# Optimization experiments

Hardware: AMD Instinct MI355X
Metric: run time of the kernel (lower is better)

The kernel has to match this reference:

```python
import jax, jax.numpy as jnp
import numpy as np

D_MODEL = 1024
NUM_HEADS = 16
D_K = D_MODEL // NUM_HEADS
LN_EPS = 1e-5


def setup_inputs() -> dict:
    key = jax.random.key(0)
    ks = jax.random.split(key, 10)
    s = 1.0 / np.sqrt(D_MODEL)
    x = jax.random.normal(ks[0], (4, 2048, D_MODEL), dtype=jnp.float32)
    Wq = jax.random.normal(ks[1], (D_MODEL, D_MODEL), dtype=jnp.float32) * s
    bq = jnp.zeros((D_MODEL,), dtype=jnp.float32)
    Wk = jax.random.normal(ks[2], (D_MODEL, D_MODEL), dtype=jnp.float32) * s
    bk = jnp.zeros((D_MODEL,), dtype=jnp.float32)
    Wv = jax.random.normal(ks[3], (D_MODEL, D_MODEL), dtype=jnp.float32) * s
    bv = jnp.zeros((D_MODEL,), dtype=jnp.float32)
    Wo = jax.random.normal(ks[4], (D_MODEL, D_MODEL), dtype=jnp.float32) * s
    bo = jnp.zeros((D_MODEL,), dtype=jnp.float32)
    gamma = jnp.ones((D_MODEL,), dtype=jnp.float32)
    beta = jnp.zeros((D_MODEL,), dtype=jnp.float32)
    return {"x": x, "Wq": Wq, "bq": bq, "Wk": Wk, "bk": bk,
            "Wv": Wv, "bv": bv, "Wo": Wo, "bo": bo,
            "gamma": gamma, "beta": beta}


def reference(x, Wq, bq, Wk, bk, Wv, bv, Wo, bo, gamma, beta):
    # x: [b, s, d]; torch Linear: y = x @ W.T + b. Dropout is identity (eval).
    b, s, d = x.shape
    h, dk = NUM_HEADS, D_K

    def proj(W, bias):  # [b, s, h, dk] -> [b, h, s, dk]
        return (jnp.einsum('bsd,ed->bse', x, W) + bias).reshape(b, s, h, dk).transpose(0, 2, 1, 3)

    Q, K, V = proj(Wq, bq), proj(Wk, bk), proj(Wv, bv)
    scores = jnp.einsum('bhqk,bhsk->bhqs', Q, K) / jnp.sqrt(jnp.float32(dk))
    attn = jax.nn.softmax(scores, axis=-1)
    ctx = jnp.einsum('bhqs,bhsk->bhqk', attn, V)  # [b, h, s, dk]
    ctx = ctx.transpose(0, 2, 1, 3).reshape(b, s, d)
    out = jnp.einsum('bsd,ed->bse', ctx, Wo) + bo
    y = out + x  # residual
    mu = jnp.mean(y, axis=-1, keepdims=True)
    var = jnp.mean(jnp.square(y - mu), axis=-1, keepdims=True)
    return (y - mu) * jax.lax.rsqrt(var + LN_EPS) * gamma + beta
```

## Files before the change

### kernel.cpp

```cpp
#include <hip/hip_runtime.h>

typedef unsigned short u16;
typedef unsigned int   u32;
typedef float f32x4 __attribute__((ext_vector_type(4)));
typedef short s16x8 __attribute__((ext_vector_type(8)));

#define D_MODEL 1024
#define NHEADS  16
#define DK      64
#define SEQ     2048
#define BATCH   4
#define MROWS   (BATCH * SEQ)

#define C2 0.18033688011112042f

#if __has_builtin(__builtin_amdgcn_exp2f)
#define EXP2(x) __builtin_amdgcn_exp2f(x)
#else
#define EXP2(x) exp2f(x)
#endif

#define GL16(gp, lp) __builtin_amdgcn_global_load_lds( \
    (const __attribute__((address_space(1))) u32*)(gp), \
    (__attribute__((address_space(3))) u32*)(lp), 16, 0, 0)

__device__ __forceinline__ u16 f2b(float f) {
    u32 u = __builtin_bit_cast(u32, f);
    u32 r = (u + 0x7fffu + ((u >> 16) & 1u)) >> 16;
    return (u16)r;
}
__device__ __forceinline__ u32 pack2_trunc(float a, float b) {
    return __builtin_amdgcn_perm(__builtin_bit_cast(u32, b),
                                 __builtin_bit_cast(u32, a), 0x07060302u);
}

__global__ __launch_bounds__(256)
void cvt_all(const float* __restrict__ x,  const float* __restrict__ wq,
             const float* __restrict__ wk, const float* __restrict__ wv,
             const float* __restrict__ wo,
             u16* __restrict__ xb, u16* __restrict__ wqb, u16* __restrict__ wkb,
             u16* __restrict__ wvb, u16* __restrict__ wob)
{
    const int i = blockIdx.x * 256 + threadIdx.x;
    const float* src; u16* dst; int off;
    if (i < 2097152) { src = x; dst = xb; off = i; }
    else {
        const int j = i - 2097152;
        const int w = j >> 18;
        off = j & 262143;
        if      (w == 0) { src = wq; dst = wqb; }
        else if (w == 1) { src = wk; dst = wkb; }
        else if (w == 2) { src = wv; dst = wvb; }
        else             { src = wo; dst = wob; }
    }
    const float4 v = reinterpret_cast<const float4*>(src)[off];
    u32 lo = (u32)f2b(v.x) | ((u32)f2b(v.y) << 16);
    u32 hi = (u32)f2b(v.z) | ((u32)f2b(v.w) << 16);
    reinterpret_cast<uint2*>(dst)[off] = make_uint2(lo, hi);
}

#define QBM 256
#define QBN 128
#define BK 32
#define KITER (D_MODEL / BK)

__global__ __launch_bounds__(512, 4)
void gemm_qkv(const u16* __restrict__ A,
              const u16* __restrict__ Wq, const u16* __restrict__ Wk,
              const u16* __restrict__ Wv,
              const float* __restrict__ bq, const float* __restrict__ bk,
              const float* __restrict__ bv,
              u16* __restrict__ Qb, u16* __restrict__ Kb, u16* __restrict__ VtB)
{
    __shared__ __align__(16) u16 As[2][8192];
    __shared__ __align__(16) u16 Bs[2][4096];
    const int t    = threadIdx.x;
    const int lane = t & 63;
    const int w    = t >> 6;
    const int wm = w >> 1, wn = w & 1;
    const int sel = blockIdx.x >> 3;
    const int n0  = (blockIdx.x & 7) * QBN;
    const int m0  = blockIdx.y * QBM;
    const int quad = lane >> 4;
    const int rlo  = lane & 15;

    const u16* W = (sel == 0) ? Wq : (sel == 1) ? Wk : Wv;
    const float* bias = (sel == 0) ? bq : (sel == 1) ? bk : bv;

    const int srow = w * 16 + rlo;
    const long aoff0 = (long)(m0 + srow) * D_MODEL + quad * 8;
    const long aoff1 = aoff0 + (long)128 * D_MODEL;
    const long boff  = (long)(n0 + srow) * D_MODEL + quad * 8;
    const int dstw = w * 512 + lane * 8;

    f32x4 acc[4][4];
    #pragma unroll
    for (int i = 0; i < 4; i++)
        #pragma unroll
        for (int j = 0; j < 4; j++)
            acc[i][j] = (f32x4){0.f, 0.f, 0.f, 0.f};

    GL16(A + aoff0, &As[0][dstw]);
    GL16(A + aoff1, &As[0][dstw + 4096]);
    GL16(W + boff,  &Bs[0][dstw]);

    for (int it = 0; it < KITER; it++) {
        const int cur = it & 1;
        __syncthreads();
        if (it + 1 < KITER) {
            const int k0 = (it + 1) * BK;
            const int nxt = cur ^ 1;
            GL16(A + aoff0 + k0, &As[nxt][dstw]);
            GL16(A + aoff1 + k0, &As[nxt][dstw + 4096]);
            GL16(W + boff + k0,  &Bs[nxt][dstw]);
        }
        s16x8 af[4], bf[4];
        #pragma unroll
        for (int i = 0; i < 4; i++)
            af[i] = *reinterpret_cast<const s16x8*>(&As[cur][(wm * 4 + i) * 512 + lane * 8]);
        #pragma unroll
        for (int j = 0; j < 4; j++)
            bf[j] = *reinterpret_cast<const s16x8*>(&Bs[cur][(wn * 4 + j) * 512 + lane * 8]);
        #pragma unroll
        for (int i = 0; i < 4; i++)
            #pragma unroll
            for (int j = 0; j < 4; j++)
                acc[i][j] = __builtin_amdgcn_mfma_f32_16x16x32_bf16(af[i], bf[j], acc[i][j], 0, 0, 0);
    }

    if (sel == 2) {
        #pragma unroll
        for (int i = 0; i < 4; i++) {
            #pragma unroll
            for (int j = 0; j < 4; j++) {
                const int gm0 = m0 + wm * 64 + i * 16 + quad * 4;
                const int gn  = n0 + wn * 64 + j * 16 + rlo;
                const float bvx = bias[gn];
                const int bb = gm0 >> 11, s = gm0 & 2047;
                const int h = gn >> 6, d = gn & 63;
                uint2 wv2;
                wv2.x = (u32)f2b(acc[i][j][0] + bvx) | ((u32)f2b(acc[i][j][1] + bvx) << 16);
                wv2.y = (u32)f2b(acc[i][j][2] + bvx) | ((u32)f2b(acc[i][j][3] + bvx) << 16);
                *reinterpret_cast<uint2*>(VtB + ((long)((bb * 16 + h) * 64 + d)) * 2048 + s) = wv2;
            }
        }
    } else {
        u16* outp = (sel == 0) ? Qb : Kb;
        const float scale = (sel == 0) ? C2 : 1.0f;
        #pragma unroll
        for (int i = 0; i < 4; i++)
            #pragma unroll
            for (int j = 0; j < 4; j++)
                #pragma unroll
                for (int r = 0; r < 4; r++) {
                    const int gm = m0 + wm * 64 + i * 16 + quad * 4 + r;
                    const int gn = n0 + wn * 64 + j * 16 + rlo;
                    outp[(long)gm * D_MODEL + gn] = f2b((acc[i][j][r] + bias[gn]) * scale);
                }
    }
}

#define BM 128
#define BN 128

__global__ __launch_bounds__(256, 3)
void gemm_o(const u16* __restrict__ A, const u16* __restrict__ W,
            const float* __restrict__ bias, const float* __restrict__ resid,
            float* __restrict__ outF)
{
    __shared__ __align__(16) u16 As[2][4096];
    __shared__ __align__(16) u16 Bs[2][4096];
    const int t    = threadIdx.x;
    const int lane = t & 63;
    const int wave = t >> 6;
    const int wr = wave >> 1, wc = wave & 1;
    const int n0  = blockIdx.x * BN;
    const int m0  = blockIdx.y * BM;
    const int quad = lane >> 4;
    const int rlo  = lane & 15;

    const int srow0 = wave * 16 + rlo;
    const int scol  = quad * 8;
    const long aoff0 = (long)(m0 + srow0) * D_MODEL + scol;
    const long aoff1 = aoff0 + (long)64 * D_MODEL;
    const long boff0 = (long)(n0 + srow0) * D_MODEL + scol;
    const long boff1 = boff0 + (long)64 * D_MODEL;
    const int dst = wave * 512 + lane * 8;

    f32x4 acc[4][4];
    #pragma unroll
    for (int i = 0; i < 4; i++)
        #pragma unroll
        for (int j = 0; j < 4; j++)
            acc[i][j] = (f32x4){0.f, 0.f, 0.f, 0.f};

    GL16(A + aoff0, &As[0][dst]);
    GL16(A + aoff1, &As[0][dst + 2048]);
    GL16(W + boff0, &Bs[0][dst]);
    GL16(W + boff1, &Bs[0][dst + 2048]);

    for (int it = 0; it < KITER; it++) {
        const int cur = it & 1;
        __syncthreads();
        if (it + 1 < KITER) {
            const int k0 = (it + 1) * BK;
            const int nxt = cur ^ 1;
            GL16(A + aoff0 + k0, &As[nxt][dst]);
            GL16(A + aoff1 + k0, &As[nxt][dst + 2048]);
            GL16(W + boff0 + k0, &Bs[nxt][dst]);
            GL16(W + boff1 + k0, &Bs[nxt][dst + 2048]);
        }
        s16x8 af[4], bf[4];
        #pragma unroll
        for (int i = 0; i < 4; i++)
            af[i] = *reinterpret_cast<const s16x8*>(&As[cur][(wr * 4 + i) * 512 + lane * 8]);
        #pragma unroll
        for (int j = 0; j < 4; j++)
            bf[j] = *reinterpret_cast<const s16x8*>(&Bs[cur][(wc * 4 + j) * 512 + lane * 8]);
        #pragma unroll
        for (int i = 0; i < 4; i++)
            #pragma unroll
            for (int j = 0; j < 4; j++)
                acc[i][j] = __builtin_amdgcn_mfma_f32_16x16x32_bf16(af[i], bf[j], acc[i][j], 0, 0, 0);
    }

    #pragma unroll
    for (int i = 0; i < 4; i++)
        #pragma unroll
        for (int j = 0; j < 4; j++)
            #pragma unroll
            for (int r = 0; r < 4; r++) {
                const int gm = m0 + wr * 64 + i * 16 + quad * 4 + r;
                const int gn = n0 + wc * 64 + j * 16 + rlo;
                outF[(long)gm * D_MODEL + gn] =
                    acc[i][j][r] + bias[gn] + resid[(long)gm * D_MODEL + gn];
            }
}

#define PSTR 72

__global__ __launch_bounds__(256, 3)
void flash_attn_mfma(const u16* __restrict__ Qg, const u16* __restrict__ Kg,
                     const u16* __restrict__ VtG, u16* __restrict__ C)
{
    __shared__ __align__(16) u16 smem[20992];
    u16* KsB   = &smem[4608];
    u16* VtBuf = &smem[12800];

    const int t    = threadIdx.x;
    const int lane = t & 63;
    const int wave = t >> 6;
    const int quad = lane >> 4;
    const int rlo  = lane & 15;
    const int qt = blockIdx.x, h = blockIdx.y, b = blockIdx.z;
    const long colbase = (long)h * DK;
    const long rowb    = (long)b * SEQ;
    const long qrow0   = rowb + (long)qt * 128;
    const u16* kg    = Kg + rowb * D_MODEL + colbase;
    const u16* vbase = VtG + (long)(b * 16 + h) * 64 * 2048;
    u16* myPs = &smem[wave * 1152];

    const long koff = (long)(wave * 16 + rlo) * D_MODEL + quad * 8;
    const long voff = (long)(wave * 16 + rlo) * 2048 + quad * 8;
    const int  dkv  = wave * 512 + lane * 8;

    GL16(kg + koff,         &KsB[dkv]);
    GL16(kg + koff + 32,    &KsB[dkv + 2048]);
    GL16(vbase + voff,      &VtBuf[dkv]);
    GL16(vbase + voff + 32, &VtBuf[dkv + 2048]);

    s16x8 bfq[2][2];
    #pragma unroll
    for (int mi = 0; mi < 2; mi++)
        #pragma unroll
        for (int ks = 0; ks < 2; ks++)
            bfq[mi][ks] = *reinterpret_cast<const s16x8*>(
                Qg + (qrow0 + wave * 32 + mi * 16 + rlo) * D_MODEL +
                colbase + ks * 32 + quad * 8);

    s16x8 ones;
    #pragma unroll
    for (int e = 0; e < 8; e++) ones[e] = (short)0x3F80;

    float m2[2] = {-INFINITY, -INFINITY};
    f32x4 o[2][4], o5[2];
    #pragma unroll
    for (int mi = 0; mi < 2; mi++) {
        o5[mi] = (f32x4){0.f, 0.f, 0.f, 0.f};
        #pragma unroll
        for (int db = 0; db < 4; db++)
            o[mi][db] = (f32x4){0.f, 0.f, 0.f, 0.f};
    }

    for (int kt = 0; kt < SEQ / 64; kt++) {
        const int cur = kt & 1;
        __syncthreads();
        if (kt + 1 < SEQ / 64) {
            const long kv0 = (long)(kt + 1) * 64;
            const int nb = cur ^ 1;
            GL16(kg + kv0 * D_MODEL + koff,      &KsB[nb * 4096 + dkv]);
            GL16(kg + kv0 * D_MODEL + koff + 32, &KsB[nb * 4096 + dkv + 2048]);
            GL16(vbase + kv0 + voff,             &VtBuf[nb * 4096 + dkv]);
            GL16(vbase + kv0 + voff + 32,        &VtBuf[nb * 4096 + dkv + 2048]);
        }
        const u16* Ks  = &KsB[cur * 4096];
        const u16* Vts = &VtBuf[cur * 4096];

        s16x8 afk[2][4], bfv[4][2];
        #pragma unroll
        for (int ks = 0; ks < 2; ks++)
            #pragma unroll
            for (int kb = 0; kb < 4; kb++)
                afk[ks][kb] = *reinterpret_cast<const s16x8*>(
                    &Ks[ks * 2048 + kb * 512 + lane * 8]);
        #pragma unroll
        for (int db = 0; db < 4; db++)
            #pragma unroll
            for (int ks = 0; ks < 2; ks++)
                bfv[db][ks] = *reinterpret_cast<const s16x8*>(
                    &Vts[ks * 2048 + db * 512 + lane * 8]);

        #pragma unroll
        for (int mi = 0; mi < 2; mi++) {
            f32x4 sc[4];
            #pragma unroll
            for (int kb = 0; kb < 4; kb++) sc[kb] = (f32x4){0.f, 0.f, 0.f, 0.f};
            #pragma unroll
            for (int ks = 0; ks < 2; ks++)
                #pragma unroll
                for (int kb = 0; kb < 4; kb++)
                    sc[kb] = __builtin_amdgcn_mfma_f32_16x16x32_bf16(
                        afk[ks][kb], bfq[mi][ks], sc[kb], 0, 0, 0);

            float rmax = sc[0][0];
            #pragma unroll
            for (int kb = 0; kb < 4; kb++)
                #pragma unroll
                for (int r = 0; r < 4; r++)
                    rmax = fmaxf(rmax, sc[kb][r]);
            rmax = fmaxf(rmax, __shfl_xor(rmax, 16));
            rmax = fmaxf(rmax, __shfl_xor(rmax, 32));
            const float mnew = fmaxf(m2[mi], rmax);
            const float alpha = EXP2(m2[mi] - mnew);
            m2[mi] = mnew;
            #pragma unroll
            for (int kb = 0; kb < 4; kb++) {
                float p0 = EXP2(sc[kb][0] - mnew);
                float p1 = EXP2(sc[kb][1] - mnew);
                float p2 = EXP2(sc[kb][2] - mnew);
                float p3 = EXP2(sc[kb][3] - mnew);
                uint2 wv2;
                wv2.x = pack2_trunc(p0, p1);
                wv2.y = pack2_trunc(p2, p3);
                *reinterpret_cast<uint2*>(&myPs[rlo * PSTR + kb * 16 + quad * 4]) = wv2;
            }

            s16x8 afp[2];
            #pragma unroll
            for (int ks = 0; ks < 2; ks++)
                afp[ks] = *reinterpret_cast<const s16x8*>(
                    &myPs[rlo * PSTR + ks * 32 + quad * 8]);

            #pragma unroll
            for (int r = 0; r < 4; r++) {
                const float ar = __shfl(alpha, (lane & 48) | (quad * 4 + r));
                #pragma unroll
                for (int db = 0; db < 4; db++)
                    o[mi][db][r] *= ar;
                o5[mi][r] *= ar;
            }

            #pragma unroll
            for (int ks = 0; ks < 2; ks++) {
                #pragma unroll
                for (int db = 0; db < 4; db++)
                    o[mi][db] = __builtin_amdgcn_mfma_f32_16x16x32_bf16(
                        afp[ks], bfv[db][ks], o[mi][db], 0, 0, 0);
                o5[mi] = __builtin_amdgcn_mfma_f32_16x16x32_bf16(
                    afp[ks], ones, o5[mi], 0, 0, 0);
            }
        }
    }

    #pragma unroll
    for (int mi = 0; mi < 2; mi++)
        #pragma unroll
        for (int r = 0; r < 4; r++) {
            const float inv = 1.f / o5[mi][r];
            const long grow = qrow0 + wave * 32 + mi * 16 + quad * 4 + r;
            #pragma unroll
            for (int db = 0; db < 4; db++)
                C[grow * D_MODEL + colbase + db * 16 + rlo] = f2b(o[mi][db][r] * inv);
        }
}

__global__ __launch_bounds__(256)
void ln_inplace(float* __restrict__ Y, const float* __restrict__ gamma,
                const float* __restrict__ beta)
{
    const int row = blockIdx.x, t = threadIdx.x;
    float4 v = reinterpret_cast<float4*>(Y + (long)row * D_MODEL)[t];
    float s  = v.x + v.y + v.z + v.w;
    float ss = v.x * v.x + v.y * v.y + v.z * v.z + v.w * v.w;
    #pragma unroll
    for (int off = 32; off > 0; off >>= 1) {
        s  += __shfl_down(s, off, 64);
        ss += __shfl_down(ss, off, 64);
    }
    __shared__ float rs[4], rss[4];
    const int lane = t & 63, w = t >> 6;
    if (lane == 0) { rs[w] = s; rss[w] = ss; }
    __syncthreads();
    const float tot  = rs[0] + rs[1] + rs[2] + rs[3];
    const float tot2 = rss[0] + rss[1] + rss[2] + rss[3];
    const float mu   = tot * (1.f / D_MODEL);
    const float var  = tot2 * (1.f / D_MODEL) - mu * mu;
    const float rstd = rsqrtf(var + 1e-5f);
    const float4 g  = reinterpret_cast<const float4*>(gamma)[t];
    const float4 bb = reinterpret_cast<const float4*>(beta)[t];
    v.x = (v.x - mu) * rstd * g.x + bb.x;
    v.y = (v.y - mu) * rstd * g.y + bb.y;
    v.z = (v.z - mu) * rstd * g.z + bb.z;
    v.w = (v.w - mu) * rstd * g.w + bb.w;
    reinterpret_cast<float4*>(Y + (long)row * D_MODEL)[t] = v;
}

extern "C" void kernel_launch(void* const* d_in, const int* in_sizes, int n_in,
                              void* d_out, int out_size, void* d_ws, size_t ws_size,
                              hipStream_t stream)
{
    const float* x     = (const float*)d_in[0];
    const float* Wq    = (const float*)d_in[1];
    const float* bq    = (const float*)d_in[2];
    const float* Wk    = (const float*)d_in[3];
    const float* bk    = (const float*)d_in[4];
    const float* Wv    = (const float*)d_in[5];
    const float* bv    = (const float*)d_in[6];
    const float* Wo    = (const float*)d_in[7];
    const float* bo    = (const float*)d_in[8];
    const float* gamma = (const float*)d_in[9];
    const float* beta  = (const float*)d_in[10];
    float* out = (float*)d_out;

    u16* ws  = (u16*)d_ws;
    u16* xb  = ws;
    u16* Wqb = xb  + (size_t)MROWS * D_MODEL;
    u16* Wkb = Wqb + (size_t)D_MODEL * D_MODEL;
    u16* Wvb = Wkb + (size_t)D_MODEL * D_MODEL;
    u16* Wob = Wvb + (size_t)D_MODEL * D_MODEL;
    u16* Qb  = Wob + (size_t)D_MODEL * D_MODEL;
    u16* Kb  = Qb  + (size_t)MROWS * D_MODEL;
    u16* VtB = Kb  + (size_t)MROWS * D_MODEL;
    u16* Cb  = VtB + (size_t)MROWS * D_MODEL;

    cvt_all<<<12288, 256, 0, stream>>>(x, Wq, Wk, Wv, Wo, xb, Wqb, Wkb, Wvb, Wob);

    gemm_qkv<<<dim3(24, 32), 512, 0, stream>>>(xb, Wqb, Wkb, Wvb, bq, bk, bv,
                                               Qb, Kb, VtB);

    flash_attn_mfma<<<dim3(SEQ / 128, NHEADS, BATCH), 256, 0, stream>>>(Qb, Kb, VtB, Cb);

    gemm_o<<<dim3(8, 64), 256, 0, stream>>>(Cb, Wob, bo, x, out);

    ln_inplace<<<MROWS, 256, 0, stream>>>(out, gamma, beta);
}
```

Baseline: 358.8 us.

## Swizzle P tile in LDS, lazy softmax rescale, setprio, raise occupancy

The padded P staging buffer (stride 72) becomes an XOR-swizzled 64-wide layout. This shrinks LDS enough to raise launch bounds from 3 to 4 blocks per SM, and each 16-byte read becomes two 8-byte reads. The online-softmax rescale of the accumulators is skipped unless some row max grows by more than 8 in log2 units, which saves multiplies and shuffles but lets unnormalized probabilities grow up to 2^8. s_setprio is also raised around the MFMA bursts to favour matrix issue across waves.

```diff
diff --git a/kernel.cpp b/kernel.cpp
--- a/kernel.cpp
+++ b/kernel.cpp
@@ -4,6 +4,7 @@
 typedef unsigned int   u32;
 typedef float f32x4 __attribute__((ext_vector_type(4)));
 typedef short s16x8 __attribute__((ext_vector_type(8)));
+typedef u32 u32x4 __attribute__((ext_vector_type(4)));
 
 #define D_MODEL 1024
 #define NHEADS  16
@@ -237,28 +238,28 @@
             }
 }
 
-#define PSTR 72
-
-__global__ __launch_bounds__(256, 3)
+
+__global__ __launch_bounds__(256, 4)
 void flash_attn_mfma(const u16* __restrict__ Qg, const u16* __restrict__ Kg,
                      const u16* __restrict__ VtG, u16* __restrict__ C)
 {
-    __shared__ __align__(16) u16 smem[20992];
-    u16* KsB   = &smem[4608];
-    u16* VtBuf = &smem[12800];
+    __shared__ __align__(16) u16 smem[20480];
+    u16* KsB   = &smem[4096];
+    u16* VtBuf = &smem[12288];
 
     const int t    = threadIdx.x;
     const int lane = t & 63;
     const int wave = t >> 6;
     const int quad = lane >> 4;
     const int rlo  = lane & 15;
+    const int swz  = rlo << 2;
     const int qt = blockIdx.x, h = blockIdx.y, b = blockIdx.z;
     const long colbase = (long)h * DK;
     const long rowb    = (long)b * SEQ;
     const long qrow0   = rowb + (long)qt * 128;
     const u16* kg    = Kg + rowb * D_MODEL + colbase;
     const u16* vbase = VtG + (long)(b * 16 + h) * 64 * 2048;
-    u16* myPs = &smem[wave * 1152];
+    u16* myPs = &smem[wave * 1024];
 
     const long koff = (long)(wave * 16 + rlo) * D_MODEL + quad * 8;
     const long voff = (long)(wave * 16 + rlo) * 2048 + quad * 8;
@@ -325,12 +326,14 @@
             f32x4 sc[4];
             #pragma unroll
             for (int kb = 0; kb < 4; kb++) sc[kb] = (f32x4){0.f, 0.f, 0.f, 0.f};
+            __builtin_amdgcn_s_setprio(1);
             #pragma unroll
             for (int ks = 0; ks < 2; ks++)
                 #pragma unroll
                 for (int kb = 0; kb < 4; kb++)
                     sc[kb] = __builtin_amdgcn_mfma_f32_16x16x32_bf16(
                         afk[ks][kb], bfq[mi][ks], sc[kb], 0, 0, 0);
+            __builtin_amdgcn_s_setprio(0);
 
             float rmax = sc[0][0];
             #pragma unroll
@@ -340,36 +343,47 @@
                     rmax = fmaxf(rmax, sc[kb][r]);
             rmax = fmaxf(rmax, __shfl_xor(rmax, 16));
             rmax = fmaxf(rmax, __shfl_xor(rmax, 32));
-            const float mnew = fmaxf(m2[mi], rmax);
-            const float alpha = EXP2(m2[mi] - mnew);
-            m2[mi] = mnew;
+
+            if (!__all(rmax <= m2[mi] + 8.0f)) {
+                const float mnew = fmaxf(m2[mi], rmax);
+                const float alpha = EXP2(m2[mi] - mnew);
+                m2[mi] = mnew;
+                #pragma unroll
+                for (int r = 0; r < 4; r++) {
+                    const float ar = __shfl(alpha, (lane & 48) | (quad * 4 + r));
+                    #pragma unroll
+                    for (int db = 0; db < 4; db++)
+                        o[mi][db][r] *= ar;
+                    o5[mi][r] *= ar;
+                }
+            }
+            const float mcur = m2[mi];
             #pragma unroll
             for (int kb = 0; kb < 4; kb++) {
-                float p0 = EXP2(sc[kb][0] - mnew);
-                float p1 = EXP2(sc[kb][1] - mnew);
-                float p2 = EXP2(sc[kb][2] - mnew);
-                float p3 = EXP2(sc[kb][3] - mnew);
+                float p0 = EXP2(sc[kb][0] - mcur);
+                float p1 = EXP2(sc[kb][1] - mcur);
+                float p2 = EXP2(sc[kb][2] - mcur);
+                float p3 = EXP2(sc[kb][3] - mcur);
                 uint2 wv2;
                 wv2.x = pack2_trunc(p0, p1);
                 wv2.y = pack2_trunc(p2, p3);
-                *reinterpret_cast<uint2*>(&myPs[rlo * PSTR + kb * 16 + quad * 4]) = wv2;
+                *reinterpret_cast<uint2*>(
+                    &myPs[rlo * 64 + ((kb * 16 + quad * 4) ^ swz)]) = wv2;
             }
 
             s16x8 afp[2];
             #pragma unroll
-            for (int ks = 0; ks < 2; ks++)
-                afp[ks] = *reinterpret_cast<const s16x8*>(
-                    &myPs[rlo * PSTR + ks * 32 + quad * 8]);
-
-            #pragma unroll
-            for (int r = 0; r < 4; r++) {
-                const float ar = __shfl(alpha, (lane & 48) | (quad * 4 + r));
-                #pragma unroll
-                for (int db = 0; db < 4; db++)
-                    o[mi][db][r] *= ar;
-                o5[mi][r] *= ar;
-            }
-
+            for (int ks = 0; ks < 2; ks++) {
+                const uint2 lo = *reinterpret_cast<const uint2*>(
+                    &myPs[rlo * 64 + ((ks * 32 + quad * 8) ^ swz)]);
+                const uint2 hi = *reinterpret_cast<const uint2*>(
+                    &myPs[rlo * 64 + ((ks * 32 + quad * 8 + 4) ^ swz)]);
+                u32x4 tv;
+                tv.x = lo.x; tv.y = lo.y; tv.z = hi.x; tv.w = hi.y;
+                afp[ks] = __builtin_bit_cast(s16x8, tv);
+            }
+
+            __builtin_amdgcn_s_setprio(1);
             #pragma unroll
             for (int ks = 0; ks < 2; ks++) {
                 #pragma unroll
@@ -379,6 +393,7 @@
                 o5[mi] = __builtin_amdgcn_mfma_f32_16x16x32_bf16(
                     afp[ks], ones, o5[mi], 0, 0, 0);
             }
+            __builtin_amdgcn_s_setprio(0);
         }
     }
 
```

Result: slower. 574.4 us (+60.1%).
